# Performance work log

Measured on AMD Instinct MI355X. Metric: run time of the kernel, lower is better.

Reference implementation:

```python
import jax, jax.numpy as jnp
import numpy as np

DIM = 512
HEADS = 8
DIM_HEAD = 64
DIM_INNER = HEADS * DIM_HEAD
SCALE = DIM_HEAD ** -0.5


def setup_inputs() -> dict:
    key = jax.random.key(0)
    ks = jax.random.split(key, 8)
    b, n = 2, 1024
    x = jax.random.normal(ks[0], (b, n, DIM), dtype=jnp.float32)
    w = lambda k, i, o: jax.random.normal(k, (i, o), dtype=jnp.float32) * 0.02
    return {
        'x': x,
        'w_q_u': w(ks[1], DIM, DIM_INNER),
        'w_k_u': w(ks[2], DIM, DIM_INNER),
        'w_v_u': w(ks[3], DIM, DIM_INNER),
        'w_q_c': w(ks[4], DIM, DIM_INNER),
        'w_k_c': w(ks[5], DIM, DIM_INNER),
        'w_v_c': w(ks[6], DIM, DIM_INNER),
        'w_out': w(ks[7], DIM_INNER, DIM),
    }


def reference(x, w_q_u, w_k_u, w_v_u, w_q_c, w_k_c, w_v_c, w_out):
    b, n, _ = x.shape

    def proj(w):  # [b,n,dim] -> [b,h,n,d]
        return (x @ w).reshape(b, n, HEADS, DIM_HEAD).transpose(0, 2, 1, 3)

    q_u, k_u, v_u = proj(w_q_u), proj(w_k_u), proj(w_v_u)
    q_c, k_c, v_c = proj(w_q_c), proj(w_k_c), proj(w_v_c)

    idx = jnp.arange(n)
    causal = idx[:, None] >= idx[None, :]  # tril ones (binary causal mask)

    # term1 = (q_c @ v_u^T) * scale, zeroed above diagonal
    term1 = jnp.einsum('bhid,bhjd->bhij', q_c, v_u) * SCALE
    term1 = term1 * causal.astype(term1.dtype)

    # sigmoid term: (q_u @ k_u^T)*scale with lookahead mask tril(-inf, diag=0)
    logits_u = jnp.einsum('bhid,bhjd->bhij', q_u, k_u) * SCALE
    sig = jax.nn.sigmoid(jnp.where(causal, -jnp.inf, logits_u))

    # S_u[i,k] = sum_j term1[i,j] * sig[k,j]
    S_u = jnp.einsum('bhij,bhkj->bhik', term1, sig)

    # S_c: causal-masked QK
    S_c = jnp.einsum('bhid,bhjd->bhij', q_c, k_c) * SCALE
    S_c = jnp.where(causal, S_c, -jnp.inf)

    final_scores = S_c - jax.nn.silu(S_u)
    attn = jax.nn.softmax(final_scores, axis=-1)
    out = jnp.einsum('bhij,bhjd->bhid', attn, v_c)  # [b,h,n,d]
    out = out.transpose(0, 2, 1, 3).reshape(b, n, DIM_INNER)
    return out @ w_out
```

## Files before the change

### kernel.cpp

```cpp
#include <hip/hip_runtime.h>
#include <math.h>


typedef __bf16 bf16x8 __attribute__((ext_vector_type(8)));
typedef float f32x4 __attribute__((ext_vector_type(4)));

#define SCALE 0.125f

#define GLL(g, l) __builtin_amdgcn_global_load_lds(                         \
    (const __attribute__((address_space(1))) void*)(g),                     \
    (__attribute__((address_space(3))) void*)(l), 16, 0, 0)

__device__ __forceinline__ unsigned short f2bf(float f){
  unsigned int x = __builtin_bit_cast(unsigned int, f);
  unsigned int r = (x + 0x7fffu + ((x >> 16) & 1u)) >> 16;
  return (unsigned short)r;
}
__device__ __forceinline__ float bf2f(unsigned short u){
  unsigned int x = ((unsigned int)u) << 16;
  return __builtin_bit_cast(float, x);
}
__device__ __forceinline__ f32x4 mfma16(bf16x8 a, bf16x8 b, f32x4 c){
  return __builtin_amdgcn_mfma_f32_16x16x32_bf16(a, b, c, 0, 0, 0);
}
__device__ __forceinline__ bf16x8 ld8(const unsigned short* p){
  return *(const bf16x8*)p;
}

__device__ const unsigned char QK_CUM[16] =
  {0,1,2,4,6,9,12,16,20,25,30,36,42,49,56,64};

__device__ const unsigned char FL_RB2[36] =
  {7, 7,6, 7,6,5, 7,6,5,4, 7,6,5,4,3, 7,6,5,4,3,2, 7,6,5,4,3,2,1,
   7,6,5,4,3,2,1,0};
__device__ const unsigned char FL_CT2[36] =
  {0, 1,0, 2,1,0, 3,2,1,0, 4,3,2,1,0, 5,4,3,2,1,0, 6,5,4,3,2,1,0,
   7,6,5,4,3,2,1,0};
__device__ const unsigned char TRI2[8] = {0,1,3,6,10,15,21,28};

__global__ __launch_bounds__(256) void k_prep(
    const float* __restrict__ x,
    const float* __restrict__ w0, const float* __restrict__ w1,
    const float* __restrict__ w2, const float* __restrict__ w3,
    const float* __restrict__ w4, const float* __restrict__ w5,
    const float* __restrict__ w6,
    unsigned short* __restrict__ xb, unsigned short* __restrict__ wT){
  int t = threadIdx.x;
  if (blockIdx.x < 576){
    for (int i = blockIdx.x * 256 + t; i < 262144; i += 576 * 256){
      float4 v = ((const float4*)x)[i];
      ushort4 o; o.x = f2bf(v.x); o.y = f2bf(v.y); o.z = f2bf(v.z); o.w = f2bf(v.w);
      ((ushort4*)xb)[i] = o;
    }
    return;
  }
  __shared__ float lds[64 * 65];
  int bx = blockIdx.x - 576;
  int mat = bx >> 6, tile = bx & 63, tr = tile >> 3, tc = tile & 7;
  int k0 = tr * 64, c0 = tc * 64;
  const float* src;
  switch (mat){
    case 0: src = w0; break; case 1: src = w1; break; case 2: src = w2; break;
    case 3: src = w3; break; case 4: src = w4; break; case 5: src = w5; break;
    default: src = w6; break;
  }
#pragma unroll
  for (int i = 0; i < 4; ++i){
    int r = (t >> 4) + i * 16, c4 = (t & 15) * 4;
    float4 v = *(const float4*)(src + (size_t)(k0 + r) * 512 + c0 + c4);
    lds[r * 65 + c4 + 0] = v.x; lds[r * 65 + c4 + 1] = v.y;
    lds[r * 65 + c4 + 2] = v.z; lds[r * 65 + c4 + 3] = v.w;
  }
  __syncthreads();
  unsigned short* dst = wT + (size_t)mat * 262144;
#pragma unroll
  for (int i = 0; i < 4; ++i){
    int oc = (t >> 4) + i * 16;
    int kq = (t & 15) * 4;
    ushort4 o;
    o.x = f2bf(lds[(kq + 0) * 65 + oc]);
    o.y = f2bf(lds[(kq + 1) * 65 + oc]);
    o.z = f2bf(lds[(kq + 2) * 65 + oc]);
    o.w = f2bf(lds[(kq + 3) * 65 + oc]);
    *(ushort4*)(dst + (size_t)(c0 + oc) * 512 + k0 + kq) = o;
  }
}

__global__ __launch_bounds__(256) void k_proj(
    const unsigned short* __restrict__ xb, const unsigned short* __restrict__ wT,
    unsigned short* __restrict__ P){
  __shared__ __align__(16) unsigned short sA[2 * 2 * 64 * 32];
  __shared__ __align__(16) unsigned short sB[2 * 2 * 128 * 32];
  int t = threadIdx.x, lane = t & 63, l16 = lane & 15, quad = lane >> 4;
  int w = t >> 6, wm = w >> 1, wn = w & 1;
  int bx = blockIdx.x;
  int mt = bx / 24, nt = bx - mt * 24;
  int M0 = mt * 64, N0 = nt * 128;
  int matb = N0 >> 9;
  int nin = N0 & 511;
  int srow = (lane >> 2), scol = (lane & 3) * 8;
  const unsigned short* gA = xb + (size_t)(M0 + w*16 + srow) * 512 + scol;
  const unsigned short* gB = wT + (size_t)matb * 262144
                               + (size_t)(nin + w*32 + srow) * 512 + scol;
  unsigned short* lA = sA + (w*16) * 32;
  unsigned short* lB = sB + (w*32) * 32;
  f32x4 acc[4][2] = {};
#define STAGE_PROJ(buf, k0) do {                                   \
    GLL(gA + (k0),               lA + (buf)*4096);                 \
    GLL(gB + (k0),               lB + (buf)*8192);                 \
    GLL(gB + (k0) + 16*512,      lB + (buf)*8192 + 16*32);         \
    GLL(gA + (k0) + 32,          lA + (buf)*4096 + 2048);          \
    GLL(gB + (k0) + 32,          lB + (buf)*8192 + 4096);          \
    GLL(gB + (k0) + 32 + 16*512, lB + (buf)*8192 + 4096 + 16*32);  \
  } while(0)
  STAGE_PROJ(0, 0);
  for (int it = 0; it < 8; ++it){
    if (it < 7){
      STAGE_PROJ((it+1) & 1, (it+1)*64);
      asm volatile("s_waitcnt vmcnt(6)" ::: "memory");
    } else {
      asm volatile("s_waitcnt vmcnt(0)" ::: "memory");
    }
    __builtin_amdgcn_s_barrier();
    int b = it & 1;
#pragma unroll
    for (int h = 0; h < 2; ++h){
      bf16x8 aw[4], ax[2];
#pragma unroll
      for (int fi = 0; fi < 4; ++fi)
        aw[fi] = *(const bf16x8*)(sB + b*8192 + h*4096 + (wn*64 + fi*16 + l16) * 32 + quad * 8);
#pragma unroll
      for (int mi = 0; mi < 2; ++mi)
        ax[mi] = *(const bf16x8*)(sA + b*4096 + h*2048 + (wm*32 + mi*16 + l16) * 32 + quad * 8);
#pragma unroll
      for (int fi = 0; fi < 4; ++fi)
#pragma unroll
        for (int mi = 0; mi < 2; ++mi)
          acc[fi][mi] = mfma16(aw[fi], ax[mi], acc[fi][mi]);
    }
    __builtin_amdgcn_s_barrier();
  }
#undef STAGE_PROJ
#pragma unroll
  for (int fi = 0; fi < 4; ++fi)
#pragma unroll
    for (int mi = 0; mi < 2; ++mi){
      int row = M0 + wm*32 + mi*16 + l16;
      int b_ = row >> 10, n_ = row & 1023;
      int c0 = N0 + wn*64 + fi*16 + quad*4;
      int h = (c0 & 511) >> 6, d = c0 & 63;
      int bh = b_*8 + h;
      ushort4 o;
      o.x = f2bf(acc[fi][mi][0]); o.y = f2bf(acc[fi][mi][1]);
      o.z = f2bf(acc[fi][mi][2]); o.w = f2bf(acc[fi][mi][3]);
      *(ushort4*)(P + (size_t)(matb*16 + bh) * 65536 + (size_t)n_ * 64 + d) = o;
    }
}

__global__ __launch_bounds__(256) void k_qk_vct(
    const unsigned short* __restrict__ P,
    unsigned short* __restrict__ term1, unsigned short* __restrict__ sig,
    unsigned short* __restrict__ vcT){
  int t = threadIdx.x;
  if (blockIdx.x < 256){
    __shared__ unsigned short lds[64 * 72];
    int bh = blockIdx.x >> 4, nt = blockIdx.x & 15;
    int N0 = nt * 64;
    const unsigned short* src = P + (size_t)(5*16 + bh) * 65536 + (size_t)N0 * 64;
#pragma unroll
    for (int i2 = 0; i2 < 2; ++i2){
      int id = i2 * 256 + t;
      int r = id >> 3, c8 = (id & 7) * 8;
      ushort4 v0 = *(const ushort4*)(src + r * 64 + c8);
      ushort4 v1 = *(const ushort4*)(src + r * 64 + c8 + 4);
      *(ushort4*)(lds + r * 72 + c8) = v0;
      *(ushort4*)(lds + r * 72 + c8 + 4) = v1;
    }
    __syncthreads();
    unsigned short* dst = vcT + (size_t)bh * 65536;
#pragma unroll
    for (int i2 = 0; i2 < 2; ++i2){
      int id = i2 * 256 + t;
      int dd = id >> 3, n8 = (id & 7) * 8;
      ushort4 a, b;
      a.x = lds[(n8+0)*72 + dd]; a.y = lds[(n8+1)*72 + dd];
      a.z = lds[(n8+2)*72 + dd]; a.w = lds[(n8+3)*72 + dd];
      b.x = lds[(n8+4)*72 + dd]; b.y = lds[(n8+5)*72 + dd];
      b.z = lds[(n8+6)*72 + dd]; b.w = lds[(n8+7)*72 + dd];
      *(ushort4*)(dst + (size_t)dd * 1024 + N0 + n8) = a;
      *(ushort4*)(dst + (size_t)dd * 1024 + N0 + n8 + 4) = b;
    }
    return;
  }
  __shared__ unsigned short sA[2 * 64 * 32], sB[2 * 128 * 32];
  int id = blockIdx.x - 256;
  int bh = id & 15, tt = id >> 4;
  int mat = (tt >= 72);
  int tl = mat ? tt - 72 : tt;
  int rb = 15;
  while (QK_CUM[rb] > tl) --rb;
  int ct = tl - QK_CUM[rb];
  int R0, C0;
  const unsigned short *Asrc, *Bsrc;
  if (!mat){ R0 = rb * 64;        C0 = ct * 128;
             Asrc = P + (size_t)(3*16 + bh) * 65536;
             Bsrc = P + (size_t)(2*16 + bh) * 65536; }
  else     { R0 = (15 - rb) * 64; C0 = (7 - ct) * 128;
             Asrc = P + (size_t)(0*16 + bh) * 65536;
             Bsrc = P + (size_t)(1*16 + bh) * 65536; }
  int lane = t & 63, l16 = lane & 15, quad = lane >> 4;
  int w = t >> 6, wm = w >> 1, wn = w & 1;
  int srow = lane >> 2, scol = (lane & 3) * 8;
  const unsigned short* gA = Asrc + (size_t)(R0 + w*16 + srow) * 64 + scol;
  const unsigned short* gB = Bsrc + (size_t)(C0 + w*32 + srow) * 64 + scol;
  unsigned short* lA0 = sA + (w*16) * 32;
  unsigned short* lB0 = sB + (w*32) * 32;
  unsigned short* lA1 = lA0 + 64 * 32;
  unsigned short* lB1 = lB0 + 128 * 32;
  f32x4 acc[4][2] = {};
  GLL(gA,              lA0);
  GLL(gB,              lB0);
  GLL(gB + 16*64,      lB0 + 16*32);
  GLL(gA + 32,         lA1);
  GLL(gB + 32,         lB1);
  GLL(gB + 32 + 16*64, lB1 + 16*32);
  __syncthreads();
#pragma unroll
  for (int h = 0; h < 2; ++h){
    bf16x8 af[2], bfr[4];
#pragma unroll
    for (int mi = 0; mi < 2; ++mi)
      af[mi] = *(const bf16x8*)(sA + h*2048 + (wm*32 + mi*16 + l16) * 32 + quad * 8);
#pragma unroll
    for (int fi = 0; fi < 4; ++fi)
      bfr[fi] = *(const bf16x8*)(sB + h*4096 + (wn*64 + fi*16 + l16) * 32 + quad * 8);
#pragma unroll
    for (int fi = 0; fi < 4; ++fi)
#pragma unroll
      for (int mi = 0; mi < 2; ++mi)
        acc[fi][mi] = mfma16(bfr[fi], af[mi], acc[fi][mi]);
  }
  unsigned short* out = (mat ? sig : term1) + (size_t)bh * 1048576;
#pragma unroll
  for (int fi = 0; fi < 4; ++fi)
#pragma unroll
    for (int mi = 0; mi < 2; ++mi){
      int row = R0 + wm*32 + mi*16 + l16;
      int c0 = C0 + wn*64 + fi*16 + quad*4;
      ushort4 o;
#pragma unroll
      for (int r = 0; r < 4; ++r){
        int col = c0 + r;
        float v = acc[fi][mi][r] * SCALE;
        unsigned short res;
        if (!mat) res = (col <= row) ? f2bf(v) : (unsigned short)0;
        else      res = (col >  row) ? f2bf(1.f / (1.f + expf(-v))) : (unsigned short)0;
        ((unsigned short*)&o)[r] = res;
      }
      *(ushort4*)(out + (size_t)row * 1024 + c0) = o;
    }
}

__global__ __launch_bounds__(512) void k_flash(
    const unsigned short* __restrict__ P,
    const unsigned short* __restrict__ term1,
    const unsigned short* __restrict__ sig,
    const unsigned short* __restrict__ vcT,
    float* __restrict__ Opart, float* __restrict__ MS){
  __shared__ __align__(16) unsigned short smem[128 * 136];
  unsigned short* sA = smem;
  unsigned short* sB = smem + 8192;
  unsigned short* probs = smem;
  float* red = (float*)smem;
  __shared__ float wpm[2][128], wps[2][128];
  int t = threadIdx.x;
  int bh = blockIdx.x & 15, q = blockIdx.x >> 4;
  int rb2 = FL_RB2[q], ct = FL_CT2[q];
  int R0 = rb2 * 128, C0 = ct * 128;
  int n_it = 2 * (rb2 + 1 - ct);
  size_t sbase = (size_t)bh * 1048576;
  int lane = t & 63, l16 = lane & 15, quad = lane >> 4, w = t >> 6;
  int wm = w >> 1, wn = w & 1;
  int srow = lane >> 3;
  int scol_sw = ((lane & 7) ^ srow) * 8;
  const unsigned short* Qc = P + (size_t)(3*16 + bh) * 65536;
  const unsigned short* Kc = P + (size_t)(4*16 + bh) * 65536;
  const unsigned short* Vt = vcT + (size_t)bh * 65536;
  const unsigned short* gA = term1 + sbase + (size_t)(R0 + w*16 + srow) * 1024 + scol_sw;
  const unsigned short* gB = sig   + sbase + (size_t)(C0 + w*16 + srow) * 1024 + scol_sw;
  unsigned short* lA = sA + (w*16) * 64;
  unsigned short* lB = sB + (w*16) * 64;
  f32x4 acc_u[4][2] = {};
  for (int it = 0; it < n_it; ++it){
    int j0 = C0 + it * 64;
    GLL(gA + j0,          lA);
    GLL(gA + j0 + 8*1024, lA + 8*64);
    GLL(gB + j0,          lB);
    GLL(gB + j0 + 8*1024, lB + 8*64);
    __syncthreads();
#pragma unroll
    for (int h = 0; h < 2; ++h){
      bf16x8 af[2], bfr[4];
#pragma unroll
      for (int mi = 0; mi < 2; ++mi){
        int row = wm*32 + mi*16 + l16;
        af[mi] = *(const bf16x8*)(sA + row*64 + ((h*32 + quad*8) ^ ((row & 7) << 3)));
      }
#pragma unroll
      for (int fi = 0; fi < 4; ++fi){
        int row = wn*64 + fi*16 + l16;
        bfr[fi] = *(const bf16x8*)(sB + row*64 + ((h*32 + quad*8) ^ ((row & 7) << 3)));
      }
#pragma unroll
      for (int fi = 0; fi < 4; ++fi)
#pragma unroll
        for (int mi = 0; mi < 2; ++mi)
          acc_u[fi][mi] = mfma16(bfr[fi], af[mi], acc_u[fi][mi]);
    }
    __syncthreads();
  }
  f32x4 acc_c[4][2] = {};
#pragma unroll
  for (int kk = 0; kk < 2; ++kk){
    bf16x8 aqk[2], bfr[4];
#pragma unroll
    for (int mi = 0; mi < 2; ++mi)
      aqk[mi] = ld8(Qc + (size_t)(R0 + wm*32 + mi*16 + l16) * 64 + kk*32 + quad*8);
#pragma unroll
    for (int fi = 0; fi < 4; ++fi)
      bfr[fi] = ld8(Kc + (size_t)(C0 + wn*64 + fi*16 + l16) * 64 + kk*32 + quad*8);
#pragma unroll
    for (int fi = 0; fi < 4; ++fi)
#pragma unroll
      for (int mi = 0; mi < 2; ++mi)
        acc_c[fi][mi] = mfma16(bfr[fi], aqk[mi], acc_c[fi][mi]);
  }
  float pm0 = -INFINITY, pm1 = -INFINITY;
#pragma unroll
  for (int fi = 0; fi < 4; ++fi)
#pragma unroll
    for (int mi = 0; mi < 2; ++mi){
      int row = R0 + wm*32 + mi*16 + l16;
      int c0 = C0 + wn*64 + fi*16 + quad*4;
#pragma unroll
      for (int r = 0; r < 4; ++r){
        float su = acc_u[fi][mi][r];
        float s = acc_c[fi][mi][r] * SCALE - su / (1.f + expf(-su));
        if (c0 + r > row) s = -INFINITY;
        acc_u[fi][mi][r] = s;
        if (mi) pm1 = fmaxf(pm1, s); else pm0 = fmaxf(pm0, s);
      }
    }
  pm0 = fmaxf(pm0, __shfl_xor(pm0, 16)); pm0 = fmaxf(pm0, __shfl_xor(pm0, 32));
  pm1 = fmaxf(pm1, __shfl_xor(pm1, 16)); pm1 = fmaxf(pm1, __shfl_xor(pm1, 32));
  if (quad == 0){
    wpm[wn][wm*32 + l16]      = pm0;
    wpm[wn][wm*32 + 16 + l16] = pm1;
  }
  __syncthreads();
  if (t < 128) wpm[0][t] = fmaxf(wpm[0][t], wpm[1][t]);
  __syncthreads();
  float mr0 = wpm[0][wm*32 + l16];
  float mr1 = wpm[0][wm*32 + 16 + l16];
  float ps0 = 0.f, ps1 = 0.f;
#pragma unroll
  for (int fi = 0; fi < 4; ++fi)
#pragma unroll
    for (int mi = 0; mi < 2; ++mi){
      ushort4 o;
#pragma unroll
      for (int r = 0; r < 4; ++r){
        float p = expf(acc_u[fi][mi][r] - (mi ? mr1 : mr0));
        if (mi) ps1 += p; else ps0 += p;
        ((unsigned short*)&o)[r] = f2bf(p);
      }
      *(ushort4*)(probs + (wm*32 + mi*16 + l16) * 136 + wn*64 + fi*16 + quad*4) = o;
    }
  ps0 += __shfl_xor(ps0, 16); ps0 += __shfl_xor(ps0, 32);
  ps1 += __shfl_xor(ps1, 16); ps1 += __shfl_xor(ps1, 32);
  if (quad == 0){
    wps[wn][wm*32 + l16]      = ps0;
    wps[wn][wm*32 + 16 + l16] = ps1;
  }
  __syncthreads();
  f32x4 acc_o[4] = {};
  const unsigned short* pr = probs + (16*w + l16) * 136 + quad * 8;
#pragma unroll
  for (int k0 = 0; k0 < 4; ++k0){
    bf16x8 a = *(const bf16x8*)(pr + k0*32);
#pragma unroll
    for (int fi = 0; fi < 4; ++fi){
      bf16x8 b = ld8(Vt + (size_t)(fi*16 + l16) * 1024 + C0 + k0*32 + quad*8);
      acc_o[fi] = mfma16(a, b, acc_o[fi]);
    }
  }
  __syncthreads();
#pragma unroll
  for (int fi = 0; fi < 4; ++fi)
#pragma unroll
    for (int r = 0; r < 4; ++r)
      red[(16*w + quad*4 + r) * 64 + fi*16 + l16] = acc_o[fi][r];
  __syncthreads();
  int slot = bh * 36 + TRI2[rb2] + ct;
#pragma unroll
  for (int pass = 0; pass < 4; ++pass){
    int e = pass * 2048 + t * 4;
    *(float4*)(Opart + (size_t)slot * 8192 + e) = *(const float4*)(red + e);
  }
  if (t < 128){
    MS[(size_t)slot * 256 + t*2]     = wpm[0][t];
    MS[(size_t)slot * 256 + t*2 + 1] = wps[0][t] + wps[1][t];
  }
}

__global__ __launch_bounds__(256) void k_comb(
    const float* __restrict__ Opart, const float* __restrict__ MS,
    unsigned short* __restrict__ O2){
  int t = threadIdx.x;
  int bh = blockIdx.x & 15, rb2 = blockIdx.x >> 4;
  int G = rb2 + 1;
  int r = t >> 1, cb = (t & 1) * 32;
  int base = bh * 36 + TRI2[rb2];
  float m = -INFINITY;
#pragma unroll
  for (int g2 = 0; g2 < 8; ++g2)
    if (g2 < G) m = fmaxf(m, MS[(size_t)(base + g2) * 256 + r*2]);
  float wg[8]; float den = 0.f;
#pragma unroll
  for (int g2 = 0; g2 < 8; ++g2){
    if (g2 < G){
      wg[g2] = expf(MS[(size_t)(base + g2) * 256 + r*2] - m);
      den += MS[(size_t)(base + g2) * 256 + r*2 + 1] * wg[g2];
    } else wg[g2] = 0.f;
  }
  float inv = 1.f / den;
  int b_ = bh >> 3, h_ = bh & 7;
#pragma unroll
  for (int c4 = 0; c4 < 8; ++c4){
    float ax = 0.f, ay = 0.f, az = 0.f, aw = 0.f;
#pragma unroll
    for (int g2 = 0; g2 < 8; ++g2){
      if (g2 < G){
        float4 v = *(const float4*)(Opart + (size_t)(base + g2) * 8192 + r*64 + cb + c4*4);
        ax += v.x * wg[g2]; ay += v.y * wg[g2];
        az += v.z * wg[g2]; aw += v.w * wg[g2];
      }
    }
    ushort4 o;
    o.x = f2bf(ax * inv); o.y = f2bf(ay * inv);
    o.z = f2bf(az * inv); o.w = f2bf(aw * inv);
    *(ushort4*)(O2 + (size_t)(b_*1024 + rb2*128 + r) * 512 + h_*64 + cb + c4*4) = o;
  }
}

__global__ __launch_bounds__(256) void k_out(
    const unsigned short* __restrict__ O2, const unsigned short* __restrict__ woT,
    float* __restrict__ out){
  __shared__ float red[4][1024];
  int t = threadIdx.x, lane = t & 63, l16 = lane & 15, quad = lane >> 4, w = t >> 6;
  int mt = blockIdx.x >> 3, nt = blockIdx.x & 7;
  int m0 = mt * 16, n0 = nt * 64;
  int r_ = m0 + l16;
  f32x4 acc[4] = {};
#pragma unroll
  for (int s = 0; s < 4; ++s){
    int kk = w * 128 + s * 32 + quad * 8;
    bf16x8 a = ld8(O2 + (size_t)r_ * 512 + kk);
#pragma unroll
    for (int fi = 0; fi < 4; ++fi){
      bf16x8 b = ld8(woT + (size_t)(n0 + fi*16 + l16) * 512 + kk);
      acc[fi] = mfma16(a, b, acc[fi]);
    }
  }
#pragma unroll
  for (int fi = 0; fi < 4; ++fi)
#pragma unroll
    for (int r = 0; r < 4; ++r)
      red[w][(quad*4 + r) * 64 + fi*16 + l16] = acc[fi][r];
  __syncthreads();
  float4 a0 = ((const float4*)red[0])[t];
  float4 a1 = ((const float4*)red[1])[t];
  float4 a2 = ((const float4*)red[2])[t];
  float4 a3 = ((const float4*)red[3])[t];
  float4 o;
  o.x = a0.x + a1.x + a2.x + a3.x;
  o.y = a0.y + a1.y + a2.y + a3.y;
  o.z = a0.z + a1.z + a2.z + a3.z;
  o.w = a0.w + a1.w + a2.w + a3.w;
  int e = t * 4, row = e >> 6, col = e & 63;
  *(float4*)(out + (size_t)(m0 + row) * 512 + n0 + col) = o;
}

extern "C" void kernel_launch(void* const* d_in, const int* in_sizes, int n_in,
                              void* d_out, int out_size, void* d_ws, size_t ws_size,
                              hipStream_t stream){
  const float* x = (const float*)d_in[0];
  float* out = (float*)d_out;
  unsigned short* ws = (unsigned short*)d_ws;

  unsigned short* wT    = ws;
  unsigned short* xb    = wT    + (size_t)7  * 262144;
  unsigned short* P     = xb    + (size_t)1048576;
  unsigned short* vcT   = P     + (size_t)96 * 65536;
  unsigned short* term1 = vcT   + (size_t)16 * 65536;
  unsigned short* sig   = term1 + (size_t)16 * 1048576;
  unsigned short* O2    = sig   + (size_t)16 * 1048576;
  unsigned short* fwsp  = O2    + (size_t)16 * 65536;
  float* Opart = (float*)fwsp;
  float* MS    = Opart + (size_t)576 * 8192;

  k_prep<<<1024, 256, 0, stream>>>(
      x,
      (const float*)d_in[1], (const float*)d_in[2], (const float*)d_in[3],
      (const float*)d_in[4], (const float*)d_in[5], (const float*)d_in[6],
      (const float*)d_in[7], xb, wT);
  k_proj<<<768, 256, 0, stream>>>(xb, wT, P);
  k_qk_vct<<<2560, 256, 0, stream>>>(P, term1, sig, vcT);
  k_flash<<<576, 512, 0, stream>>>(P, term1, sig, vcT, Opart, MS);
  k_comb<<<128, 256, 0, stream>>>(Opart, MS, O2);
  k_out<<<1024, 256, 0, stream>>>(O2, wT + (size_t)6 * 262144, out);
}
```

Baseline: 181.8 us.

## Fuse term1 and sigmoid score computation into flash kernel, dropping materialized matrices

After: 259.3 us. 1.43x slower.

```diff
diff --git a/kernel.cpp b/kernel.cpp
--- a/kernel.cpp
+++ b/kernel.cpp
@@ -26,9 +26,6 @@
 __device__ __forceinline__ bf16x8 ld8(const unsigned short* p){
   return *(const bf16x8*)p;
 }
-
-__device__ const unsigned char QK_CUM[16] =
-  {0,1,2,4,6,9,12,16,20,25,30,36,42,49,56,64};
 
 __device__ const unsigned char FL_RB2[36] =
   {7, 7,6, 7,6,5, 7,6,5,4, 7,6,5,4,3, 7,6,5,4,3,2, 7,6,5,4,3,2,1,
@@ -157,119 +154,45 @@
     }
 }
 
-__global__ __launch_bounds__(256) void k_qk_vct(
-    const unsigned short* __restrict__ P,
-    unsigned short* __restrict__ term1, unsigned short* __restrict__ sig,
-    unsigned short* __restrict__ vcT){
+__global__ __launch_bounds__(256) void k_vct(
+    const unsigned short* __restrict__ P, unsigned short* __restrict__ vcT){
   int t = threadIdx.x;
-  if (blockIdx.x < 256){
-    __shared__ unsigned short lds[64 * 72];
-    int bh = blockIdx.x >> 4, nt = blockIdx.x & 15;
-    int N0 = nt * 64;
-    const unsigned short* src = P + (size_t)(5*16 + bh) * 65536 + (size_t)N0 * 64;
-#pragma unroll
-    for (int i2 = 0; i2 < 2; ++i2){
-      int id = i2 * 256 + t;
-      int r = id >> 3, c8 = (id & 7) * 8;
-      ushort4 v0 = *(const ushort4*)(src + r * 64 + c8);
-      ushort4 v1 = *(const ushort4*)(src + r * 64 + c8 + 4);
-      *(ushort4*)(lds + r * 72 + c8) = v0;
-      *(ushort4*)(lds + r * 72 + c8 + 4) = v1;
-    }
-    __syncthreads();
-    unsigned short* dst = vcT + (size_t)bh * 65536;
-#pragma unroll
-    for (int i2 = 0; i2 < 2; ++i2){
-      int id = i2 * 256 + t;
-      int dd = id >> 3, n8 = (id & 7) * 8;
-      ushort4 a, b;
-      a.x = lds[(n8+0)*72 + dd]; a.y = lds[(n8+1)*72 + dd];
-      a.z = lds[(n8+2)*72 + dd]; a.w = lds[(n8+3)*72 + dd];
-      b.x = lds[(n8+4)*72 + dd]; b.y = lds[(n8+5)*72 + dd];
-      b.z = lds[(n8+6)*72 + dd]; b.w = lds[(n8+7)*72 + dd];
-      *(ushort4*)(dst + (size_t)dd * 1024 + N0 + n8) = a;
-      *(ushort4*)(dst + (size_t)dd * 1024 + N0 + n8 + 4) = b;
-    }
-    return;
-  }
-  __shared__ unsigned short sA[2 * 64 * 32], sB[2 * 128 * 32];
-  int id = blockIdx.x - 256;
-  int bh = id & 15, tt = id >> 4;
-  int mat = (tt >= 72);
-  int tl = mat ? tt - 72 : tt;
-  int rb = 15;
-  while (QK_CUM[rb] > tl) --rb;
-  int ct = tl - QK_CUM[rb];
-  int R0, C0;
-  const unsigned short *Asrc, *Bsrc;
-  if (!mat){ R0 = rb * 64;        C0 = ct * 128;
-             Asrc = P + (size_t)(3*16 + bh) * 65536;
-             Bsrc = P + (size_t)(2*16 + bh) * 65536; }
-  else     { R0 = (15 - rb) * 64; C0 = (7 - ct) * 128;
-             Asrc = P + (size_t)(0*16 + bh) * 65536;
-             Bsrc = P + (size_t)(1*16 + bh) * 65536; }
-  int lane = t & 63, l16 = lane & 15, quad = lane >> 4;
-  int w = t >> 6, wm = w >> 1, wn = w & 1;
-  int srow = lane >> 2, scol = (lane & 3) * 8;
-  const unsigned short* gA = Asrc + (size_t)(R0 + w*16 + srow) * 64 + scol;
-  const unsigned short* gB = Bsrc + (size_t)(C0 + w*32 + srow) * 64 + scol;
-  unsigned short* lA0 = sA + (w*16) * 32;
-  unsigned short* lB0 = sB + (w*32) * 32;
-  unsigned short* lA1 = lA0 + 64 * 32;
-  unsigned short* lB1 = lB0 + 128 * 32;
-  f32x4 acc[4][2] = {};
-  GLL(gA,              lA0);
-  GLL(gB,              lB0);
-  GLL(gB + 16*64,      lB0 + 16*32);
-  GLL(gA + 32,         lA1);
-  GLL(gB + 32,         lB1);
-  GLL(gB + 32 + 16*64, lB1 + 16*32);
-  __syncthreads();
-#pragma unroll
-  for (int h = 0; h < 2; ++h){
-    bf16x8 af[2], bfr[4];
-#pragma unroll
-    for (int mi = 0; mi < 2; ++mi)
-      af[mi] = *(const bf16x8*)(sA + h*2048 + (wm*32 + mi*16 + l16) * 32 + quad * 8);
-#pragma unroll
-    for (int fi = 0; fi < 4; ++fi)
-      bfr[fi] = *(const bf16x8*)(sB + h*4096 + (wn*64 + fi*16 + l16) * 32 + quad * 8);
-#pragma unroll
-    for (int fi = 0; fi < 4; ++fi)
-#pragma unroll
-      for (int mi = 0; mi < 2; ++mi)
-        acc[fi][mi] = mfma16(bfr[fi], af[mi], acc[fi][mi]);
-  }
-  unsigned short* out = (mat ? sig : term1) + (size_t)bh * 1048576;
-#pragma unroll
-  for (int fi = 0; fi < 4; ++fi)
-#pragma unroll
-    for (int mi = 0; mi < 2; ++mi){
-      int row = R0 + wm*32 + mi*16 + l16;
-      int c0 = C0 + wn*64 + fi*16 + quad*4;
-      ushort4 o;
-#pragma unroll
-      for (int r = 0; r < 4; ++r){
-        int col = c0 + r;
-        float v = acc[fi][mi][r] * SCALE;
-        unsigned short res;
-        if (!mat) res = (col <= row) ? f2bf(v) : (unsigned short)0;
-        else      res = (col >  row) ? f2bf(1.f / (1.f + expf(-v))) : (unsigned short)0;
-        ((unsigned short*)&o)[r] = res;
-      }
-      *(ushort4*)(out + (size_t)row * 1024 + c0) = o;
-    }
+  __shared__ unsigned short lds[64 * 72];
+  int bh = blockIdx.x >> 4, nt = blockIdx.x & 15;
+  int N0 = nt * 64;
+  const unsigned short* src = P + (size_t)(5*16 + bh) * 65536 + (size_t)N0 * 64;
+#pragma unroll
+  for (int i2 = 0; i2 < 2; ++i2){
+    int id = i2 * 256 + t;
+    int r = id >> 3, c8 = (id & 7) * 8;
+    ushort4 v0 = *(const ushort4*)(src + r * 64 + c8);
+    ushort4 v1 = *(const ushort4*)(src + r * 64 + c8 + 4);
+    *(ushort4*)(lds + r * 72 + c8) = v0;
+    *(ushort4*)(lds + r * 72 + c8 + 4) = v1;
+  }
+  __syncthreads();
+  unsigned short* dst = vcT + (size_t)bh * 65536;
+#pragma unroll
+  for (int i2 = 0; i2 < 2; ++i2){
+    int id = i2 * 256 + t;
+    int dd = id >> 3, n8 = (id & 7) * 8;
+    ushort4 a, b;
+    a.x = lds[(n8+0)*72 + dd]; a.y = lds[(n8+1)*72 + dd];
+    a.z = lds[(n8+2)*72 + dd]; a.w = lds[(n8+3)*72 + dd];
+    b.x = lds[(n8+4)*72 + dd]; b.y = lds[(n8+5)*72 + dd];
+    b.z = lds[(n8+6)*72 + dd]; b.w = lds[(n8+7)*72 + dd];
+    *(ushort4*)(dst + (size_t)dd * 1024 + N0 + n8) = a;
+    *(ushort4*)(dst + (size_t)dd * 1024 + N0 + n8 + 4) = b;
+  }
 }
 
 __global__ __launch_bounds__(512) void k_flash(
     const unsigned short* __restrict__ P,
-    const unsigned short* __restrict__ term1,
-    const unsigned short* __restrict__ sig,
     const unsigned short* __restrict__ vcT,
     float* __restrict__ Opart, float* __restrict__ MS){
-  __shared__ __align__(16) unsigned short smem[128 * 136];
-  unsigned short* sA = smem;
-  unsigned short* sB = smem + 8192;
+  __shared__ __align__(16) unsigned short smem[2 * 128 * 72];
+  unsigned short* Tlds = smem;
+  unsigned short* Glds = smem + 128 * 72;
   unsigned short* probs = smem;
   float* red = (float*)smem;
   __shared__ float wpm[2][128], wps[2][128];
@@ -278,44 +201,70 @@
   int rb2 = FL_RB2[q], ct = FL_CT2[q];
   int R0 = rb2 * 128, C0 = ct * 128;
   int n_it = 2 * (rb2 + 1 - ct);
-  size_t sbase = (size_t)bh * 1048576;
   int lane = t & 63, l16 = lane & 15, quad = lane >> 4, w = t >> 6;
   int wm = w >> 1, wn = w & 1;
-  int srow = lane >> 3;
-  int scol_sw = ((lane & 7) ^ srow) * 8;
+  const unsigned short* Qu = P + (size_t)(0*16 + bh) * 65536;
+  const unsigned short* Ku = P + (size_t)(1*16 + bh) * 65536;
+  const unsigned short* Vu = P + (size_t)(2*16 + bh) * 65536;
   const unsigned short* Qc = P + (size_t)(3*16 + bh) * 65536;
   const unsigned short* Kc = P + (size_t)(4*16 + bh) * 65536;
   const unsigned short* Vt = vcT + (size_t)bh * 65536;
-  const unsigned short* gA = term1 + sbase + (size_t)(R0 + w*16 + srow) * 1024 + scol_sw;
-  const unsigned short* gB = sig   + sbase + (size_t)(C0 + w*16 + srow) * 1024 + scol_sw;
-  unsigned short* lA = sA + (w*16) * 64;
-  unsigned short* lB = sB + (w*16) * 64;
+  bf16x8 aqT[2], aqU[2];
+#pragma unroll
+  for (int kk = 0; kk < 2; ++kk){
+    aqT[kk] = ld8(Qc + (size_t)(R0 + w*16 + l16) * 64 + kk*32 + quad*8);
+    aqU[kk] = ld8(Qu + (size_t)(C0 + w*16 + l16) * 64 + kk*32 + quad*8);
+  }
+  int irow = R0 + w*16 + l16;
+  int krow = C0 + w*16 + l16;
   f32x4 acc_u[4][2] = {};
   for (int it = 0; it < n_it; ++it){
-    int j0 = C0 + it * 64;
-    GLL(gA + j0,          lA);
-    GLL(gA + j0 + 8*1024, lA + 8*64);
-    GLL(gB + j0,          lB);
-    GLL(gB + j0 + 8*1024, lB + 8*64);
+    int jb = C0 + it * 64;
+    f32x4 accT[4] = {}, accG[4] = {};
+#pragma unroll
+    for (int kk = 0; kk < 2; ++kk){
+      bf16x8 bv[4], bk[4];
+#pragma unroll
+      for (int fi = 0; fi < 4; ++fi){
+        bv[fi] = ld8(Vu + (size_t)(jb + fi*16 + l16) * 64 + kk*32 + quad*8);
+        bk[fi] = ld8(Ku + (size_t)(jb + fi*16 + l16) * 64 + kk*32 + quad*8);
+      }
+#pragma unroll
+      for (int fi = 0; fi < 4; ++fi){
+        accT[fi] = mfma16(bv[fi], aqT[kk], accT[fi]);
+        accG[fi] = mfma16(bk[fi], aqU[kk], accG[fi]);
+      }
+    }
+#pragma unroll
+    for (int fi = 0; fi < 4; ++fi){
+      ushort4 oT, oG;
+#pragma unroll
+      for (int r = 0; r < 4; ++r){
+        int col = jb + fi*16 + quad*4 + r;
+        float tv = accT[fi][r] * SCALE;
+        ((unsigned short*)&oT)[r] = (col <= irow) ? f2bf(tv) : (unsigned short)0;
+        float gv = accG[fi][r] * SCALE;
+        ((unsigned short*)&oG)[r] =
+            (col > krow) ? f2bf(1.f / (1.f + expf(-gv))) : (unsigned short)0;
+      }
+      *(ushort4*)(Tlds + (w*16 + l16) * 72 + fi*16 + quad*4) = oT;
+      *(ushort4*)(Glds + (w*16 + l16) * 72 + fi*16 + quad*4) = oG;
+    }
     __syncthreads();
 #pragma unroll
-    for (int h = 0; h < 2; ++h){
-      bf16x8 af[2], bfr[4];
-#pragma unroll
-      for (int mi = 0; mi < 2; ++mi){
-        int row = wm*32 + mi*16 + l16;
-        af[mi] = *(const bf16x8*)(sA + row*64 + ((h*32 + quad*8) ^ ((row & 7) << 3)));
-      }
-#pragma unroll
-      for (int fi = 0; fi < 4; ++fi){
-        int row = wn*64 + fi*16 + l16;
-        bfr[fi] = *(const bf16x8*)(sB + row*64 + ((h*32 + quad*8) ^ ((row & 7) << 3)));
-      }
+    for (int kk = 0; kk < 2; ++kk){
+      bf16x8 tf[2], gf[4];
+#pragma unroll
+      for (int mi = 0; mi < 2; ++mi)
+        tf[mi] = *(const bf16x8*)(Tlds + (wm*32 + mi*16 + l16) * 72 + kk*32 + quad*8);
 #pragma unroll
       for (int fi = 0; fi < 4; ++fi)
+        gf[fi] = *(const bf16x8*)(Glds + (wn*64 + fi*16 + l16) * 72 + kk*32 + quad*8);
+#pragma unroll
+      for (int fi = 0; fi < 4; ++fi)
 #pragma unroll
         for (int mi = 0; mi < 2; ++mi)
-          acc_u[fi][mi] = mfma16(bfr[fi], af[mi], acc_u[fi][mi]);
+          acc_u[fi][mi] = mfma16(gf[fi], tf[mi], acc_u[fi][mi]);
     }
     __syncthreads();
   }
@@ -502,9 +451,7 @@
   unsigned short* xb    = wT    + (size_t)7  * 262144;
   unsigned short* P     = xb    + (size_t)1048576;
   unsigned short* vcT   = P     + (size_t)96 * 65536;
-  unsigned short* term1 = vcT   + (size_t)16 * 65536;
-  unsigned short* sig   = term1 + (size_t)16 * 1048576;
-  unsigned short* O2    = sig   + (size_t)16 * 1048576;
+  unsigned short* O2    = vcT   + (size_t)16 * 65536;
   unsigned short* fwsp  = O2    + (size_t)16 * 65536;
   float* Opart = (float*)fwsp;
   float* MS    = Opart + (size_t)576 * 8192;
@@ -515,8 +462,8 @@
       (const float*)d_in[4], (const float*)d_in[5], (const float*)d_in[6],
       (const float*)d_in[7], xb, wT);
   k_proj<<<768, 256, 0, stream>>>(xb, wT, P);
-  k_qk_vct<<<2560, 256, 0, stream>>>(P, term1, sig, vcT);
-  k_flash<<<576, 512, 0, stream>>>(P, term1, sig, vcT, Opart, MS);
+  k_vct<<<256, 256, 0, stream>>>(P, vcT);
+  k_flash<<<576, 512, 0, stream>>>(P, vcT, Opart, MS);
   k_comb<<<128, 256, 0, stream>>>(Opart, MS, O2);
   k_out<<<1024, 256, 0, stream>>>(O2, wT + (size_t)6 * 262144, out);
 }
```
